# Kernel optimization log

Measured on AMD Instinct MI355X. Metric: run time of the kernel, lower is better.

## Reference

```python
import jax, jax.numpy as jnp
import numpy as np

B, S, D = 4, 512, 256
VOCAB, MAX_RULES = 50257, 1024
EPS = 1e-12  # F.normalize default eps


def setup_inputs() -> dict:
    key = jax.random.key(0)
    k1, k2, k3, k4 = jax.random.split(key, 4)
    hidden_states = jax.random.normal(k1, (B, S, D), dtype=jnp.float32)
    token_ids = jax.random.randint(k2, (B, S), 0, VOCAB, dtype=jnp.int64)
    rule_transform = jax.random.normal(k3, (MAX_RULES, D, D), dtype=jnp.float32)
    token_rules = jax.random.randint(k4, (VOCAB,), 0, MAX_RULES, dtype=jnp.int64)
    return {
        "hidden_states": hidden_states,
        "token_ids": token_ids,
        "rule_transform": rule_transform,
        "token_rules": token_rules,
    }


def reference(hidden_states, token_ids, rule_transform, token_rules):
    # per-token rule index: [B, S]
    rule_indices = token_rules[token_ids]
    # gather DxD rule matrix per token: [B, S, D, D]
    rule_matrices = rule_transform[rule_indices]
    # F.normalize(p=2, dim=(-2,-1)): divide by Frobenius norm per matrix
    fro = jnp.sqrt(jnp.sum(rule_matrices * rule_matrices, axis=(-2, -1), keepdims=True))
    rule_matrices = rule_matrices / jnp.maximum(fro, EPS)
    # batched matvec: [B,S,D] x [B,S,D,E] -> [B,S,E]
    return jnp.einsum("bsd,bsde->bse", hidden_states, rule_matrices)
```

## Files before the change

kernel.cpp:

```cpp
#include <hip/hip_runtime.h>
#include <math.h>

#define D 256
#define NRULES 1024
#define TPB 4


__global__ void zero_counts_kernel(int* __restrict__ counts) {
    counts[threadIdx.x + blockIdx.x * blockDim.x] = 0;
}

__global__ void count_kernel(const int* __restrict__ token_ids,
                             const int* __restrict__ token_rules,
                             int* __restrict__ counts,
                             int* __restrict__ rule_of_token,
                             int ntok) {
    const int i = threadIdx.x + blockIdx.x * blockDim.x;
    if (i >= ntok) return;
    const int r = token_rules[token_ids[i]];
    rule_of_token[i] = r;
    atomicAdd(&counts[r], 1);
}

__global__ __launch_bounds__(NRULES) void scan_kernel(
    const int* __restrict__ counts,
    int* __restrict__ starts,
    int* __restrict__ cursor) {
    __shared__ int tmp[NRULES];
    const int t = threadIdx.x;
    const int v = counts[t];
    tmp[t] = v;
    __syncthreads();
    #pragma unroll
    for (int off = 1; off < NRULES; off <<= 1) {
        const int add = (t >= off) ? tmp[t - off] : 0;
        __syncthreads();
        tmp[t] += add;
        __syncthreads();
    }
    const int incl = tmp[t];
    const int excl = incl - v;
    starts[t] = excl;
    cursor[t] = excl;
    if (t == NRULES - 1) starts[NRULES] = incl;
}

__global__ void scatter_kernel(const int* __restrict__ rule_of_token,
                               int* __restrict__ cursor,
                               int* __restrict__ bucket,
                               int ntok) {
    const int i = threadIdx.x + blockIdx.x * blockDim.x;
    if (i >= ntok) return;
    const int r = rule_of_token[i];
    const int pos = atomicAdd(&cursor[r], 1);
    bucket[pos] = i;
}


__global__ __launch_bounds__(256) void process_kernel(
    const float* __restrict__ hidden,
    const float* __restrict__ rules,
    const int*   __restrict__ starts,
    const int*   __restrict__ bucket,
    float* __restrict__ out)
{
    const int r     = blockIdx.x;
    const int start = starts[r];
    const int count = starts[r + 1] - start;
    if (count <= 0) return;

    const int t    = threadIdx.x;
    const int wave = t >> 6;
    const int lane = t & 63;

    __shared__ float h_lds[TPB][D];
    __shared__ float y_lds[TPB][4][D];
    __shared__ float sq_lds[4];
    __shared__ int   toks[TPB];

    const float* __restrict__ M = rules + (size_t)r * D * D;
    const int d0  = wave << 6;
    const int col = lane << 2;

    for (int base = 0; base < count; base += TPB) {
        if (t < TPB)
            toks[t] = (base + t < count) ? bucket[start + base + t] : -1;
        #pragma unroll
        for (int j = 0; j < TPB; ++j) {
            const int idx = base + j;
            h_lds[j][t] = (idx < count)
                ? hidden[(size_t)bucket[start + idx] * D + t] : 0.f;
        }
        __syncthreads();

        float4 acc[TPB];
        #pragma unroll
        for (int j = 0; j < TPB; ++j) acc[j] = float4{0.f, 0.f, 0.f, 0.f};
        float sq = 0.f;

        #pragma unroll 4
        for (int i = 0; i < 64; ++i) {
            const int d = d0 + i;
            const float4 m = *reinterpret_cast<const float4*>(M + (size_t)d * D + col);
            sq = fmaf(m.x, m.x, fmaf(m.y, m.y, fmaf(m.z, m.z, fmaf(m.w, m.w, sq))));
            #pragma unroll
            for (int j = 0; j < TPB; ++j) {
                const float h = h_lds[j][d];
                acc[j].x = fmaf(h, m.x, acc[j].x);
                acc[j].y = fmaf(h, m.y, acc[j].y);
                acc[j].z = fmaf(h, m.z, acc[j].z);
                acc[j].w = fmaf(h, m.w, acc[j].w);
            }
        }

        #pragma unroll
        for (int off = 32; off > 0; off >>= 1)
            sq += __shfl_down(sq, off, 64);
        if (lane == 0) sq_lds[wave] = sq;

        #pragma unroll
        for (int j = 0; j < TPB; ++j)
            *reinterpret_cast<float4*>(&y_lds[j][wave][col]) = acc[j];
        __syncthreads();

        const float fro2 = sq_lds[0] + sq_lds[1] + sq_lds[2] + sq_lds[3];
        const float inv  = 1.0f / fmaxf(sqrtf(fro2), 1e-12f);

        #pragma unroll
        for (int j = 0; j < TPB; ++j) {
            const int tok = toks[j];
            if (tok >= 0) {
                const float v = (y_lds[j][0][t] + y_lds[j][1][t] +
                                 y_lds[j][2][t] + y_lds[j][3][t]) * inv;
                out[(size_t)tok * D + t] = v;
            }
        }
        __syncthreads();
    }
}


extern "C" void kernel_launch(void* const* d_in, const int* in_sizes, int n_in,
                              void* d_out, int out_size, void* d_ws, size_t ws_size,
                              hipStream_t stream) {
    const float* hidden      = (const float*)d_in[0];
    const int*   token_ids   = (const int*)d_in[1];
    const float* rules       = (const float*)d_in[2];
    const int*   token_rules = (const int*)d_in[3];
    float*       out         = (float*)d_out;

    const int ntok = in_sizes[1];

    int* ws            = (int*)d_ws;
    int* counts        = ws;
    int* starts        = ws + NRULES;
    int* cursor        = ws + 2 * NRULES + 8;
    int* rule_of_token = ws + 3 * NRULES + 16;
    int* bucket        = rule_of_token + ntok;

    zero_counts_kernel<<<NRULES / 256, 256, 0, stream>>>(counts);
    count_kernel<<<(ntok + 255) / 256, 256, 0, stream>>>(
        token_ids, token_rules, counts, rule_of_token, ntok);
    scan_kernel<<<1, NRULES, 0, stream>>>(counts, starts, cursor);
    scatter_kernel<<<(ntok + 255) / 256, 256, 0, stream>>>(
        rule_of_token, cursor, bucket, ntok);
    process_kernel<<<NRULES, 256, 0, stream>>>(
        hidden, rules, starts, bucket, out);
}
```

Measured before the change: 61.34 us.

## Fuse bucketing into one shared-memory prep kernel and compact the rule worklist

```diff
diff --git a/kernel.cpp b/kernel.cpp
--- a/kernel.cpp
+++ b/kernel.cpp
@@ -4,70 +4,79 @@
 #define D 256
 #define NRULES 1024
 #define TPB 4
+#define NTOK_MAX 4096
 
+__global__ __launch_bounds__(1024) void prep_kernel(
+    const int* __restrict__ token_ids,
+    const int* __restrict__ token_rules,
+    int ntok,
+    int* __restrict__ starts,
+    int* __restrict__ bucket,
+    int* __restrict__ worklist,
+    int* __restrict__ nwork)
+{
+    __shared__ int cnt[NRULES];
+    __shared__ int rtok[NTOK_MAX];
+    __shared__ int wl[NRULES];
+    __shared__ int nw;
 
-__global__ void zero_counts_kernel(int* __restrict__ counts) {
-    counts[threadIdx.x + blockIdx.x * blockDim.x] = 0;
-}
+    const int t = threadIdx.x;
+    cnt[t] = 0;
+    if (t == 0) nw = 0;
+    __syncthreads();
 
-__global__ void count_kernel(const int* __restrict__ token_ids,
-                             const int* __restrict__ token_rules,
-                             int* __restrict__ counts,
-                             int* __restrict__ rule_of_token,
-                             int ntok) {
-    const int i = threadIdx.x + blockIdx.x * blockDim.x;
-    if (i >= ntok) return;
-    const int r = token_rules[token_ids[i]];
-    rule_of_token[i] = r;
-    atomicAdd(&counts[r], 1);
-}
+    for (int i = t; i < ntok; i += 1024) {
+        const int r = token_rules[token_ids[i]];
+        rtok[i] = r;
+        atomicAdd(&cnt[r], 1);
+    }
+    __syncthreads();
 
-__global__ __launch_bounds__(NRULES) void scan_kernel(
-    const int* __restrict__ counts,
-    int* __restrict__ starts,
-    int* __restrict__ cursor) {
-    __shared__ int tmp[NRULES];
-    const int t = threadIdx.x;
-    const int v = counts[t];
-    tmp[t] = v;
-    __syncthreads();
+    const int c = cnt[t];
+
     #pragma unroll
     for (int off = 1; off < NRULES; off <<= 1) {
-        const int add = (t >= off) ? tmp[t - off] : 0;
+        const int add = (t >= off) ? cnt[t - off] : 0;
         __syncthreads();
-        tmp[t] += add;
+        cnt[t] += add;
         __syncthreads();
     }
-    const int incl = tmp[t];
-    const int excl = incl - v;
+    const int incl = cnt[t];
+    const int excl = incl - c;
     starts[t] = excl;
-    cursor[t] = excl;
     if (t == NRULES - 1) starts[NRULES] = incl;
+
+    if (c > TPB) wl[atomicAdd(&nw, 1)] = t;
+    __syncthreads();
+    if (c > 0 && c <= TPB) wl[atomicAdd(&nw, 1)] = t;
+
+    __syncthreads();
+    cnt[t] = excl;
+    __syncthreads();
+
+    for (int i = t; i < ntok; i += 1024) {
+        const int pos = atomicAdd(&cnt[rtok[i]], 1);
+        bucket[pos] = i;
+    }
+
+    const int nwv = nw;
+    for (int i = t; i < nwv; i += 1024) worklist[i] = wl[i];
+    if (t == 0) nwork[0] = nwv;
 }
-
-__global__ void scatter_kernel(const int* __restrict__ rule_of_token,
-                               int* __restrict__ cursor,
-                               int* __restrict__ bucket,
-                               int ntok) {
-    const int i = threadIdx.x + blockIdx.x * blockDim.x;
-    if (i >= ntok) return;
-    const int r = rule_of_token[i];
-    const int pos = atomicAdd(&cursor[r], 1);
-    bucket[pos] = i;
-}
-
 
 __global__ __launch_bounds__(256) void process_kernel(
     const float* __restrict__ hidden,
     const float* __restrict__ rules,
     const int*   __restrict__ starts,
     const int*   __restrict__ bucket,
+    const int*   __restrict__ worklist,
+    const int*   __restrict__ nwork,
     float* __restrict__ out)
 {
-    const int r     = blockIdx.x;
+    if ((int)blockIdx.x >= nwork[0]) return;
+    const int r     = worklist[blockIdx.x];
     const int start = starts[r];
     const int count = starts[r + 1] - start;
-    if (count <= 0) return;
 
     const int t    = threadIdx.x;
     const int wave = t >> 6;
@@ -139,7 +148,6 @@
     }
 }
 
-
 extern "C" void kernel_launch(void* const* d_in, const int* in_sizes, int n_in,
                               void* d_out, int out_size, void* d_ws, size_t ws_size,
                               hipStream_t stream) {
@@ -151,19 +159,14 @@
 
     const int ntok = in_sizes[1];
 
-    int* ws            = (int*)d_ws;
-    int* counts        = ws;
-    int* starts        = ws + NRULES;
-    int* cursor        = ws + 2 * NRULES + 8;
-    int* rule_of_token = ws + 3 * NRULES + 16;
-    int* bucket        = rule_of_token + ntok;
+    int* ws       = (int*)d_ws;
+    int* starts   = ws;
+    int* bucket   = starts + NRULES + 8;
+    int* worklist = bucket + ntok;
+    int* nwork    = worklist + NRULES;
 
-    zero_counts_kernel<<<NRULES / 256, 256, 0, stream>>>(counts);
-    count_kernel<<<(ntok + 255) / 256, 256, 0, stream>>>(
-        token_ids, token_rules, counts, rule_of_token, ntok);
-    scan_kernel<<<1, NRULES, 0, stream>>>(counts, starts, cursor);
-    scatter_kernel<<<(ntok + 255) / 256, 256, 0, stream>>>(
-        rule_of_token, cursor, bucket, ntok);
+    prep_kernel<<<1, 1024, 0, stream>>>(
+        token_ids, token_rules, ntok, starts, bucket, worklist, nwork);
     process_kernel<<<NRULES, 256, 0, stream>>>(
-        hidden, rules, starts, bucket, out);
+        hidden, rules, starts, bucket, worklist, nwork, out);
 }
```

New measurement: 54.97 us. -10.4%, faster.
